# Optimization experiments

Hardware: AMD Instinct MI355X
Metric: run time of the kernel (lower is better)

Reference implementation:

```python
import jax, jax.numpy as jnp
import numpy as np

B, LQ, LK, D = 32, 1024, 1024, 256

def setup_inputs() -> dict:
    key = jax.random.key(0)
    ks = jax.random.split(key, 7)
    return {
        "raw_query": jax.random.normal(ks[0], (B, LQ, D), dtype=jnp.float32),
        "raw_key": jax.random.normal(ks[1], (B, LK, D), dtype=jnp.float32),
        "raw_value": jax.random.normal(ks[2], (B, LK, D), dtype=jnp.float32),
        "value_mask": jax.random.randint(ks[3], (B, LQ), 0, 2, dtype=jnp.int32),
        "WQ": jax.random.normal(ks[4], (D, D), dtype=jnp.float32) * 0.05,
        "WK": jax.random.normal(ks[5], (D, D), dtype=jnp.float32) * 0.05,
        "WV": jax.random.normal(ks[6], (D, D), dtype=jnp.float32) * 0.05,
    }

def reference(raw_query, raw_key, raw_value, value_mask, WQ, WK, WV):
    # Projections: [B, L, D] @ [D, D]
    Q = raw_query @ WQ
    K = raw_key @ WK
    V = raw_value @ WV
    # Scores: [B, LQ, LK] (use_scale=False -> no 1/sqrt(d_k))
    att = jnp.einsum("bqd,bkd->bqk", Q, K)
    # Mask expanded on axis=2 -> zeroes entire query rows of scores (faithful to tf.where+zeros_like)
    att = jnp.where(value_mask[:, :, None] > 0, att, jnp.zeros((), dtype=att.dtype))
    att = jax.nn.softmax(att, axis=-1)
    # Output: [B, LQ, D]
    return jnp.einsum("bqk,bkd->bqd", att, V)
```

## Files before the change

### kernel.cpp

```cpp
#include <hip/hip_runtime.h>
#include <hip/hip_bf16.h>
#include <math.h>

#define B_ 32
#define L_ 1024
#define D_ 256

typedef _Float16 half8 __attribute__((ext_vector_type(8)));
typedef __fp16   fp16x2 __attribute__((ext_vector_type(2)));
typedef short    s16x8 __attribute__((ext_vector_type(8)));
typedef float    f32x4 __attribute__((ext_vector_type(4)));

typedef __attribute__((address_space(3))) unsigned int lds_u32;
typedef __attribute__((address_space(1))) unsigned int gbl_u32;

__device__ __forceinline__ void gl_lds16(const void* g, void* l) {
    __builtin_amdgcn_global_load_lds((gbl_u32*)g, (lds_u32*)l, 16, 0, 0);
}

__device__ __forceinline__ unsigned short f2bf(float x) {
    unsigned u = __float_as_uint(x);
    u += 0x7FFFu + ((u >> 16) & 1u);
    return (unsigned short)(u >> 16);
}

__device__ __forceinline__ unsigned short f2h(float x) {
    _Float16 h = (_Float16)x;
    unsigned short u;
    __builtin_memcpy(&u, &h, 2);
    return u;
}

__device__ __forceinline__ unsigned pkrtz(float a, float b) {
    fp16x2 v = __builtin_amdgcn_cvt_pkrtz(a, b);
    unsigned u;
    __builtin_memcpy(&u, &v, 4);
    return u;
}

__global__ __launch_bounds__(256) void wprep_kernel(
    const float* __restrict__ W0, const float* __restrict__ W1,
    const float* __restrict__ W2, unsigned short* __restrict__ Wt)
{
    const int z = blockIdx.z;
    const float* __restrict__ W = (z == 0) ? W0 : (z == 1) ? W1 : W2;
    __shared__ unsigned short T[64][72];
    const int k0 = blockIdx.x << 6, n0 = blockIdx.y << 6;
    const int t = threadIdx.x;
    const int r = t >> 2, c0 = (t & 3) << 4;
    #pragma unroll
    for (int j = 0; j < 16; j += 4) {
        float4 w4 = *(const float4*)(W + (size_t)(k0 + r) * 256 + n0 + c0 + j);
        T[c0 + j + 0][r] = f2h(w4.x);
        T[c0 + j + 1][r] = f2h(w4.y);
        T[c0 + j + 2][r] = f2h(w4.z);
        T[c0 + j + 3][r] = f2h(w4.w);
    }
    __syncthreads();
    const int n = t >> 2, kc = (t & 3) << 4;
    unsigned short* dst = Wt + ((size_t)z << 16) + (size_t)(n0 + n) * 256 + k0 + kc;
    *(uint4*)(dst + 0) = *(const uint4*)&T[n][kc + 0];
    *(uint4*)(dst + 8) = *(const uint4*)&T[n][kc + 8];
}

__global__ __launch_bounds__(256) void proj_mfma_kernel(
    const float* __restrict__ A0, const float* __restrict__ A1,
    const float* __restrict__ A2, const unsigned short* __restrict__ Wt,
    unsigned short* __restrict__ Qh, unsigned short* __restrict__ Kh,
    unsigned short* __restrict__ Vt)
{
    __shared__ unsigned short SMEM[32768];
    unsigned short* Asm = SMEM;
    unsigned short* Bsm = SMEM + 16384;

    const int z = blockIdx.z;
    const float* __restrict__ A = (z == 0) ? A0 : (z == 1) ? A1 : A2;
    const int bm = blockIdx.x << 7, bn = blockIdx.y << 7;
    const int t = threadIdx.x, lane = t & 63, w = t >> 6;
    const int wm = (w >> 1) << 6, wn = (w & 1) << 6;

    const float* __restrict__ Ag = A + (size_t)bm * 256;
    const unsigned short* __restrict__ Bg = Wt + ((size_t)z << 16) + (size_t)bn * 256;

    f32x4 acc[4][4];
    const f32x4 z4 = {0.f, 0.f, 0.f, 0.f};
    #pragma unroll
    for (int mi = 0; mi < 4; ++mi)
        #pragma unroll
        for (int ni = 0; ni < 4; ++ni) acc[mi][ni] = z4;

    float4 a_reg[8];

    auto loadA = [&](int it) {
        #pragma unroll
        for (int i = 0; i < 8; ++i) {
            int r  = (t >> 4) + (i << 4);
            int c4 = t & 15;
            a_reg[i] = *(const float4*)(Ag + (size_t)r * 256 + (it << 6) + (c4 << 2));
        }
    };
    auto writeA = [&](int buf) {
        #pragma unroll
        for (int i = 0; i < 8; ++i) {
            int r  = (t >> 4) + (i << 4);
            int c4 = t & 15;
            unsigned h01 = pkrtz(a_reg[i].x, a_reg[i].y);
            unsigned h23 = pkrtz(a_reg[i].z, a_reg[i].w);
            int cs = (c4 >> 1) ^ (r & 7);
            uint2 d2; d2.x = h01; d2.y = h23;
            *(uint2*)&Asm[(buf << 13) + (r << 6) + (cs << 3) + ((c4 & 1) << 2)] = d2;
        }
    };
    auto stageB = [&](int buf, int it) {
        #pragma unroll
        for (int rr = 0; rr < 4; ++rr) {
            int o = (rr << 8) + t;
            int r = o >> 3, c = o & 7;
            int cs = c ^ (r & 7);
            gl_lds16(Bg + (size_t)r * 256 + (it << 6) + (cs << 3),
                     &Bsm[(buf << 13) + (o << 3)]);
        }
    };
    auto compute = [&](int buf) {
        #pragma unroll
        for (int kc = 0; kc < 2; ++kc) {
            half8 af[4], bfr[4];
            #pragma unroll
            for (int mi = 0; mi < 4; ++mi) {
                int m = wm + (mi << 4) + (lane & 15);
                int cs = ((kc << 2) + (lane >> 4)) ^ (m & 7);
                af[mi] = *(const half8*)&Asm[(buf << 13) + (m << 6) + (cs << 3)];
            }
            #pragma unroll
            for (int ni = 0; ni < 4; ++ni) {
                int n = wn + (ni << 4) + (lane & 15);
                int cs = ((kc << 2) + (lane >> 4)) ^ (n & 7);
                bfr[ni] = *(const half8*)&Bsm[(buf << 13) + (n << 6) + (cs << 3)];
            }
            #pragma unroll
            for (int mi = 0; mi < 4; ++mi)
                #pragma unroll
                for (int ni = 0; ni < 4; ++ni)
                    acc[mi][ni] = __builtin_amdgcn_mfma_f32_16x16x32_f16(
                        af[mi], bfr[ni], acc[mi][ni], 0, 0, 0);
        }
    };

    loadA(0);
    writeA(0);
    stageB(0, 0);
    loadA(1);
    __syncthreads();

    for (int it = 0; it < 4; ++it) {
        const int buf = it & 1;
        if (it < 3) {
            stageB(buf ^ 1, it + 1);
            writeA(buf ^ 1);
            if (it < 2) loadA(it + 2);
        }
        compute(buf);
        __syncthreads();
    }

    if (z < 2) {
        unsigned short* __restrict__ C = (z == 0) ? Qh : Kh;
        #pragma unroll
        for (int mi = 0; mi < 4; ++mi) {
            int q = bm + wm + (mi << 4) + ((lane >> 4) << 2);
            #pragma unroll
            for (int ni = 0; ni < 4; ++ni) {
                int col = bn + wn + (ni << 4) + (lane & 15);
                #pragma unroll
                for (int r = 0; r < 4; ++r)
                    C[(size_t)(q + r) * 256 + col] = f2h(acc[mi][ni][r]);
            }
        }
    } else {
        __syncthreads();
        unsigned short (*Tt)[144] = (unsigned short(*)[144])SMEM;
        #pragma unroll
        for (int mi = 0; mi < 4; ++mi) {
            #pragma unroll
            for (int ni = 0; ni < 4; ++ni) {
                int n  = wn + (ni << 4) + (lane & 15);
                int m0 = wm + (mi << 4) + ((lane >> 4) << 2);
                ushort4 v;
                v.x = f2bf(acc[mi][ni][0]);
                v.y = f2bf(acc[mi][ni][1]);
                v.z = f2bf(acc[mi][ni][2]);
                v.w = f2bf(acc[mi][ni][3]);
                *(ushort4*)&Tt[n][m0] = v;
            }
        }
        __syncthreads();
        const int bb = bm >> 10, kin = bm & 1023;
        const int dr = t >> 1, cb = (t & 1) << 6;
        unsigned short* dst = Vt + ((size_t)bb * 256 + bn + dr) * 1024 + kin + cb;
        #pragma unroll
        for (int j = 0; j < 8; ++j)
            *(uint4*)(dst + (j << 3)) = *(const uint4*)&Tt[dr][cb + (j << 3)];
    }
}

__global__ __launch_bounds__(512, 2) void fused_attn_kernel(
    const unsigned short* __restrict__ Qh, const unsigned short* __restrict__ Kh,
    const unsigned short* __restrict__ Vt, const int* __restrict__ mask,
    float* __restrict__ Out)
{
    __shared__ unsigned short Ks[2][16384];
    __shared__ unsigned short Vs[2][16384];
    __shared__ unsigned short Ps[9216];
    __shared__ float lred[128][2];

    const int b = blockIdx.y, q0 = blockIdx.x << 7;
    const size_t bL = (size_t)b * L_;
    const int t = threadIdx.x, lane = t & 63, w = t >> 6;
    const int wm_s = (w >> 1) << 5, wn_s = (w & 1) << 5;
    const int wm_v = (w >> 2) << 6, wn_v = (w & 3) << 6;

    const unsigned short* __restrict__ Kb = Kh + (bL << 8);
    const unsigned short* __restrict__ Vb = Vt + (bL << 8);

    auto stageK = [&](int buf, int kt) {
        #pragma unroll
        for (int i = 0; i < 4; ++i) {
            int o = (i << 9) + t;
            int r = o >> 5, c = o & 31;
            int cs = (c & 24) | ((c & 7) ^ (r & 7));
            gl_lds16(Kb + (size_t)((kt << 6) + r) * 256 + (cs << 3), &Ks[buf][o << 3]);
        }
    };
    auto stageV = [&](int buf, int kt) {
        #pragma unroll
        for (int i = 0; i < 4; ++i) {
            int o = (i << 9) + t;
            int d = o >> 3, c = o & 7;
            int cs = c ^ (d & 7);
            gl_lds16(Vb + ((size_t)d << 10) + (kt << 6) + (cs << 3), &Vs[buf][o << 3]);
        }
    };

    stageK(0, 0);
    stageV(0, 0);

    half8 qf[2][8];
    #pragma unroll
    for (int mi = 0; mi < 2; ++mi) {
        int m = wm_s + (mi << 4) + (lane & 15);
        const unsigned short* qp = Qh + ((bL + q0 + m) << 8) + ((lane >> 4) << 3);
        #pragma unroll
        for (int kc = 0; kc < 8; ++kc)
            qf[mi][kc] = *(const half8*)(qp + (kc << 5));
    }
    int mv[2][4];
    #pragma unroll
    for (int mi = 0; mi < 2; ++mi)
        #pragma unroll
        for (int r = 0; r < 4; ++r)
            mv[mi][r] = mask[bL + q0 + wm_s + (mi << 4) + ((lane >> 4) << 2) + r];

    f32x4 o_acc[4][4];
    const f32x4 z4 = {0.f, 0.f, 0.f, 0.f};
    #pragma unroll
    for (int mi = 0; mi < 4; ++mi)
        #pragma unroll
        for (int ni = 0; ni < 4; ++ni) o_acc[mi][ni] = z4;
    float lacc[2][4] = {};

    __syncthreads();

    for (int kt = 0; kt < 16; ++kt) {
        const int cur = kt & 1;
        if (kt < 15) { stageK(cur ^ 1, kt + 1); stageV(cur ^ 1, kt + 1); }

        f32x4 accs[2][2];
        accs[0][0] = z4; accs[0][1] = z4; accs[1][0] = z4; accs[1][1] = z4;
        #pragma unroll
        for (int kc = 0; kc < 8; ++kc) {
            int kb = (kc >> 1) << 6, cc = ((kc & 1) << 2) + (lane >> 4);
            int n0 = wn_s + (lane & 15);
            int n1 = n0 + 16;
            half8 bf0 = *(const half8*)&Ks[cur][(n0 << 8) + kb + ((cc ^ (n0 & 7)) << 3)];
            half8 bf1 = *(const half8*)&Ks[cur][(n1 << 8) + kb + ((cc ^ (n1 & 7)) << 3)];
            accs[0][0] = __builtin_amdgcn_mfma_f32_16x16x32_f16(qf[0][kc], bf0, accs[0][0], 0, 0, 0);
            accs[1][0] = __builtin_amdgcn_mfma_f32_16x16x32_f16(qf[1][kc], bf0, accs[1][0], 0, 0, 0);
            accs[0][1] = __builtin_amdgcn_mfma_f32_16x16x32_f16(qf[0][kc], bf1, accs[0][1], 0, 0, 0);
            accs[1][1] = __builtin_amdgcn_mfma_f32_16x16x32_f16(qf[1][kc], bf1, accs[1][1], 0, 0, 0);
        }

        #pragma unroll
        for (int mi = 0; mi < 2; ++mi) {
            int qrow = wm_s + (mi << 4) + ((lane >> 4) << 2);
            #pragma unroll
            for (int ni = 0; ni < 2; ++ni) {
                int kl = wn_s + (ni << 4) + (lane & 15);
                #pragma unroll
                for (int r = 0; r < 4; ++r) {
                    float p = mv[mi][r] ? __expf(accs[mi][ni][r]) : 1.0f;
                    Ps[(qrow + r) * 72 + kl] = f2bf(p);
                    lacc[mi][r] += p;
                }
            }
        }
        __syncthreads();

        #pragma unroll
        for (int kc2 = 0; kc2 < 2; ++kc2) {
            s16x8 pa[4], vb[4];
            #pragma unroll
            for (int mi = 0; mi < 4; ++mi) {
                int m = wm_v + (mi << 4) + (lane & 15);
                pa[mi] = *(const s16x8*)&Ps[m * 72 + (kc2 << 5) + ((lane >> 4) << 3)];
            }
            #pragma unroll
            for (int ni = 0; ni < 4; ++ni) {
                int n = wn_v + (ni << 4) + (lane & 15);
                int cc = (kc2 << 2) + (lane >> 4);
                vb[ni] = *(const s16x8*)&Vs[cur][(n << 6) + ((cc ^ (n & 7)) << 3)];
            }
            #pragma unroll
            for (int mi = 0; mi < 4; ++mi)
                #pragma unroll
                for (int ni = 0; ni < 4; ++ni)
                    o_acc[mi][ni] = __builtin_amdgcn_mfma_f32_16x16x32_bf16(
                        pa[mi], vb[ni], o_acc[mi][ni], 0, 0, 0);
        }
        __syncthreads();
    }

    #pragma unroll
    for (int mi = 0; mi < 2; ++mi)
        #pragma unroll
        for (int r = 0; r < 4; ++r) {
            float v = lacc[mi][r];
            v += __shfl_xor(v, 1);
            v += __shfl_xor(v, 2);
            v += __shfl_xor(v, 4);
            v += __shfl_xor(v, 8);
            if ((lane & 15) == 0)
                lred[wm_s + (mi << 4) + ((lane >> 4) << 2) + r][w & 1] = v;
        }
    __syncthreads();

    #pragma unroll
    for (int mi = 0; mi < 4; ++mi) {
        #pragma unroll
        for (int rr = 0; rr < 4; ++rr) {
            int q = wm_v + (mi << 4) + ((lane >> 4) << 2) + rr;
            float inv = 1.0f / (lred[q][0] + lred[q][1]);
            #pragma unroll
            for (int ni = 0; ni < 4; ++ni) {
                int d = wn_v + (ni << 4) + (lane & 15);
                Out[((bL + q0 + q) << 8) + d] = o_acc[mi][ni][rr] * inv;
            }
        }
    }
}

extern "C" void kernel_launch(void* const* d_in, const int* in_sizes, int n_in,
                              void* d_out, int out_size, void* d_ws, size_t ws_size,
                              hipStream_t stream) {
    const float* rq = (const float*)d_in[0];
    const float* rk = (const float*)d_in[1];
    const float* rv = (const float*)d_in[2];
    const int*   vm = (const int*)d_in[3];
    const float* WQ = (const float*)d_in[4];
    const float* WK = (const float*)d_in[5];
    const float* WV = (const float*)d_in[6];
    float* out = (float*)d_out;

    char* ws = (char*)d_ws;
    unsigned short* Qh = (unsigned short*)(ws);
    unsigned short* Kh = (unsigned short*)(ws + ((size_t)16 << 20));
    unsigned short* Vt = (unsigned short*)(ws + ((size_t)32 << 20));
    unsigned short* Wt = (unsigned short*)(ws + ((size_t)48 << 20));

    dim3 wg(4, 4, 3);
    wprep_kernel<<<wg, 256, 0, stream>>>(WQ, WK, WV, Wt);

    dim3 pg(256, 2, 3);
    proj_mfma_kernel<<<pg, 256, 0, stream>>>(rq, rk, rv, Wt, Qh, Kh, Vt);

    dim3 fg(8, 32);
    fused_attn_kernel<<<fg, 512, 0, stream>>>(Qh, Kh, Vt, vm, out);
}
```

Baseline: 98.43 us.

## Halve query tile, single-buffer K/V with split staging, remap grid for occupancy

```diff
diff --git a/kernel.cpp b/kernel.cpp
--- a/kernel.cpp
+++ b/kernel.cpp
@@ -203,113 +203,112 @@
     }
 }
 
-__global__ __launch_bounds__(512, 2) void fused_attn_kernel(
+__global__ __launch_bounds__(512, 4) void fused_attn_kernel(
     const unsigned short* __restrict__ Qh, const unsigned short* __restrict__ Kh,
     const unsigned short* __restrict__ Vt, const int* __restrict__ mask,
     float* __restrict__ Out)
 {
-    __shared__ unsigned short Ks[2][16384];
-    __shared__ unsigned short Vs[2][16384];
-    __shared__ unsigned short Ps[9216];
-    __shared__ float lred[128][2];
-
-    const int b = blockIdx.y, q0 = blockIdx.x << 7;
+    __shared__ unsigned short Ks[16384];
+    __shared__ unsigned short Vs[16384];
+    __shared__ unsigned short Ps[64 * 72];
+    __shared__ float lred[64][2];
+
+    const int f  = blockIdx.x;
+    const int b  = (f & 7) + ((f >> 7) << 3);
+    const int q0 = ((f >> 3) & 15) << 6;
     const size_t bL = (size_t)b * L_;
     const int t = threadIdx.x, lane = t & 63, w = t >> 6;
-    const int wm_s = (w >> 1) << 5, wn_s = (w & 1) << 5;
-    const int wm_v = (w >> 2) << 6, wn_v = (w & 3) << 6;
+    const int wm_s = (w >> 1) << 4, wn_s = (w & 1) << 5;
+    const int wm_v = (w >> 2) << 5, wn_v = (w & 3) << 6;
 
     const unsigned short* __restrict__ Kb = Kh + (bL << 8);
     const unsigned short* __restrict__ Vb = Vt + (bL << 8);
 
-    auto stageK = [&](int buf, int kt) {
+    auto stageK = [&](int kt) {
         #pragma unroll
         for (int i = 0; i < 4; ++i) {
             int o = (i << 9) + t;
             int r = o >> 5, c = o & 31;
             int cs = (c & 24) | ((c & 7) ^ (r & 7));
-            gl_lds16(Kb + (size_t)((kt << 6) + r) * 256 + (cs << 3), &Ks[buf][o << 3]);
-        }
-    };
-    auto stageV = [&](int buf, int kt) {
+            gl_lds16(Kb + (size_t)((kt << 6) + r) * 256 + (cs << 3), &Ks[o << 3]);
+        }
+    };
+    auto stageV = [&](int kt) {
         #pragma unroll
         for (int i = 0; i < 4; ++i) {
             int o = (i << 9) + t;
             int d = o >> 3, c = o & 7;
             int cs = c ^ (d & 7);
-            gl_lds16(Vb + ((size_t)d << 10) + (kt << 6) + (cs << 3), &Vs[buf][o << 3]);
-        }
-    };
-
-    stageK(0, 0);
-    stageV(0, 0);
-
-    half8 qf[2][8];
-    #pragma unroll
-    for (int mi = 0; mi < 2; ++mi) {
-        int m = wm_s + (mi << 4) + (lane & 15);
+            gl_lds16(Vb + ((size_t)d << 10) + (kt << 6) + (cs << 3), &Vs[o << 3]);
+        }
+    };
+
+    stageK(0);
+    stageV(0);
+
+    half8 qf[8];
+    {
+        int m = wm_s + (lane & 15);
         const unsigned short* qp = Qh + ((bL + q0 + m) << 8) + ((lane >> 4) << 3);
         #pragma unroll
         for (int kc = 0; kc < 8; ++kc)
-            qf[mi][kc] = *(const half8*)(qp + (kc << 5));
-    }
-    int mv[2][4];
+            qf[kc] = *(const half8*)(qp + (kc << 5));
+    }
+    int mv[4];
+    {
+        int qrow = wm_s + ((lane >> 4) << 2);
+        #pragma unroll
+        for (int r = 0; r < 4; ++r) mv[r] = mask[bL + q0 + qrow + r];
+    }
+
+    f32x4 o_acc[2][4];
+    const f32x4 z4 = {0.f, 0.f, 0.f, 0.f};
     #pragma unroll
     for (int mi = 0; mi < 2; ++mi)
         #pragma unroll
-        for (int r = 0; r < 4; ++r)
-            mv[mi][r] = mask[bL + q0 + wm_s + (mi << 4) + ((lane >> 4) << 2) + r];
-
-    f32x4 o_acc[4][4];
-    const f32x4 z4 = {0.f, 0.f, 0.f, 0.f};
-    #pragma unroll
-    for (int mi = 0; mi < 4; ++mi)
-        #pragma unroll
         for (int ni = 0; ni < 4; ++ni) o_acc[mi][ni] = z4;
-    float lacc[2][4] = {};
+    float lacc[4] = {};
 
     __syncthreads();
 
     for (int kt = 0; kt < 16; ++kt) {
-        const int cur = kt & 1;
-        if (kt < 15) { stageK(cur ^ 1, kt + 1); stageV(cur ^ 1, kt + 1); }
-
-        f32x4 accs[2][2];
-        accs[0][0] = z4; accs[0][1] = z4; accs[1][0] = z4; accs[1][1] = z4;
+        if (kt > 0) stageV(kt);
+
+        f32x4 accs[2];
+        accs[0] = z4; accs[1] = z4;
         #pragma unroll
         for (int kc = 0; kc < 8; ++kc) {
             int kb = (kc >> 1) << 6, cc = ((kc & 1) << 2) + (lane >> 4);
             int n0 = wn_s + (lane & 15);
             int n1 = n0 + 16;
-            half8 bf0 = *(const half8*)&Ks[cur][(n0 << 8) + kb + ((cc ^ (n0 & 7)) << 3)];
-            half8 bf1 = *(const half8*)&Ks[cur][(n1 << 8) + kb + ((cc ^ (n1 & 7)) << 3)];
-            accs[0][0] = __builtin_amdgcn_mfma_f32_16x16x32_f16(qf[0][kc], bf0, accs[0][0], 0, 0, 0);
-            accs[1][0] = __builtin_amdgcn_mfma_f32_16x16x32_f16(qf[1][kc], bf0, accs[1][0], 0, 0, 0);
-            accs[0][1] = __builtin_amdgcn_mfma_f32_16x16x32_f16(qf[0][kc], bf1, accs[0][1], 0, 0, 0);
-            accs[1][1] = __builtin_amdgcn_mfma_f32_16x16x32_f16(qf[1][kc], bf1, accs[1][1], 0, 0, 0);
-        }
-
-        #pragma unroll
-        for (int mi = 0; mi < 2; ++mi) {
-            int qrow = wm_s + (mi << 4) + ((lane >> 4) << 2);
+            half8 bf0 = *(const half8*)&Ks[(n0 << 8) + kb + ((cc ^ (n0 & 7)) << 3)];
+            half8 bf1 = *(const half8*)&Ks[(n1 << 8) + kb + ((cc ^ (n1 & 7)) << 3)];
+            accs[0] = __builtin_amdgcn_mfma_f32_16x16x32_f16(qf[kc], bf0, accs[0], 0, 0, 0);
+            accs[1] = __builtin_amdgcn_mfma_f32_16x16x32_f16(qf[kc], bf1, accs[1], 0, 0, 0);
+        }
+
+        {
+            int qrow = wm_s + ((lane >> 4) << 2);
             #pragma unroll
             for (int ni = 0; ni < 2; ++ni) {
                 int kl = wn_s + (ni << 4) + (lane & 15);
                 #pragma unroll
                 for (int r = 0; r < 4; ++r) {
-                    float p = mv[mi][r] ? __expf(accs[mi][ni][r]) : 1.0f;
+                    float p = mv[r] ? __expf(accs[ni][r]) : 1.0f;
                     Ps[(qrow + r) * 72 + kl] = f2bf(p);
-                    lacc[mi][r] += p;
+                    lacc[r] += p;
                 }
             }
         }
         __syncthreads();
 
+        if (kt < 15) stageK(kt + 1);
+
         #pragma unroll
         for (int kc2 = 0; kc2 < 2; ++kc2) {
-            s16x8 pa[4], vb[4];
-            #pragma unroll
-            for (int mi = 0; mi < 4; ++mi) {
+            s16x8 pa[2], vb[4];
+            #pragma unroll
+            for (int mi = 0; mi < 2; ++mi) {
                 int m = wm_v + (mi << 4) + (lane & 15);
                 pa[mi] = *(const s16x8*)&Ps[m * 72 + (kc2 << 5) + ((lane >> 4) << 3)];
             }
@@ -317,10 +316,10 @@
             for (int ni = 0; ni < 4; ++ni) {
                 int n = wn_v + (ni << 4) + (lane & 15);
                 int cc = (kc2 << 2) + (lane >> 4);
-                vb[ni] = *(const s16x8*)&Vs[cur][(n << 6) + ((cc ^ (n & 7)) << 3)];
-            }
-            #pragma unroll
-            for (int mi = 0; mi < 4; ++mi)
+                vb[ni] = *(const s16x8*)&Vs[(n << 6) + ((cc ^ (n & 7)) << 3)];
+            }
+            #pragma unroll
+            for (int mi = 0; mi < 2; ++mi)
                 #pragma unroll
                 for (int ni = 0; ni < 4; ++ni)
                     o_acc[mi][ni] = __builtin_amdgcn_mfma_f32_16x16x32_bf16(
@@ -330,21 +329,19 @@
     }
 
     #pragma unroll
-    for (int mi = 0; mi < 2; ++mi)
-        #pragma unroll
-        for (int r = 0; r < 4; ++r) {
-            float v = lacc[mi][r];
-            v += __shfl_xor(v, 1);
-            v += __shfl_xor(v, 2);
-            v += __shfl_xor(v, 4);
-            v += __shfl_xor(v, 8);
-            if ((lane & 15) == 0)
-                lred[wm_s + (mi << 4) + ((lane >> 4) << 2) + r][w & 1] = v;
-        }
+    for (int r = 0; r < 4; ++r) {
+        float v = lacc[r];
+        v += __shfl_xor(v, 1);
+        v += __shfl_xor(v, 2);
+        v += __shfl_xor(v, 4);
+        v += __shfl_xor(v, 8);
+        if ((lane & 15) == 0)
+            lred[wm_s + ((lane >> 4) << 2) + r][w & 1] = v;
+    }
     __syncthreads();
 
     #pragma unroll
-    for (int mi = 0; mi < 4; ++mi) {
+    for (int mi = 0; mi < 2; ++mi) {
         #pragma unroll
         for (int rr = 0; rr < 4; ++rr) {
             int q = wm_v + (mi << 4) + ((lane >> 4) << 2) + rr;
@@ -382,6 +379,5 @@
     dim3 pg(256, 2, 3);
     proj_mfma_kernel<<<pg, 256, 0, stream>>>(rq, rk, rv, Wt, Qh, Kh, Vt);
 
-    dim3 fg(8, 32);
-    fused_attn_kernel<<<fg, 512, 0, stream>>>(Qh, Kh, Vt, vm, out);
-}
+    fused_attn_kernel<<<512, 512, 0, stream>>>(Qh, Kh, Vt, vm, out);
+}
```

After: 100.6 us. 2.2% more time.

## Single-buffer K/V tiles, swizzle P tile, remap grid for XCD locality

Applied to the files above, without the earlier changes.

```diff
diff --git a/kernel.cpp b/kernel.cpp
--- a/kernel.cpp
+++ b/kernel.cpp
@@ -203,17 +203,19 @@
     }
 }
 
-__global__ __launch_bounds__(512, 2) void fused_attn_kernel(
+__global__ __launch_bounds__(512, 4) void fused_attn_kernel(
     const unsigned short* __restrict__ Qh, const unsigned short* __restrict__ Kh,
     const unsigned short* __restrict__ Vt, const int* __restrict__ mask,
     float* __restrict__ Out)
 {
-    __shared__ unsigned short Ks[2][16384];
-    __shared__ unsigned short Vs[2][16384];
-    __shared__ unsigned short Ps[9216];
-    __shared__ float lred[128][2];
-
-    const int b = blockIdx.y, q0 = blockIdx.x << 7;
+    __shared__ unsigned short Ks[16384];
+    __shared__ unsigned short Vs[16384];
+    __shared__ unsigned short Ps[128 * 64];
+    float* lredp = (float*)Ps;
+
+    const int f  = blockIdx.x;
+    const int b  = (f & 7) + ((f >> 6) << 3);
+    const int q0 = ((f >> 3) & 7) << 7;
     const size_t bL = (size_t)b * L_;
     const int t = threadIdx.x, lane = t & 63, w = t >> 6;
     const int wm_s = (w >> 1) << 5, wn_s = (w & 1) << 5;
@@ -222,27 +224,27 @@
     const unsigned short* __restrict__ Kb = Kh + (bL << 8);
     const unsigned short* __restrict__ Vb = Vt + (bL << 8);
 
-    auto stageK = [&](int buf, int kt) {
+    auto stageK = [&](int kt) {
         #pragma unroll
         for (int i = 0; i < 4; ++i) {
             int o = (i << 9) + t;
             int r = o >> 5, c = o & 31;
             int cs = (c & 24) | ((c & 7) ^ (r & 7));
-            gl_lds16(Kb + (size_t)((kt << 6) + r) * 256 + (cs << 3), &Ks[buf][o << 3]);
-        }
-    };
-    auto stageV = [&](int buf, int kt) {
+            gl_lds16(Kb + (size_t)((kt << 6) + r) * 256 + (cs << 3), &Ks[o << 3]);
+        }
+    };
+    auto stageV = [&](int kt) {
         #pragma unroll
         for (int i = 0; i < 4; ++i) {
             int o = (i << 9) + t;
             int d = o >> 3, c = o & 7;
             int cs = c ^ (d & 7);
-            gl_lds16(Vb + ((size_t)d << 10) + (kt << 6) + (cs << 3), &Vs[buf][o << 3]);
-        }
-    };
-
-    stageK(0, 0);
-    stageV(0, 0);
+            gl_lds16(Vb + ((size_t)d << 10) + (kt << 6) + (cs << 3), &Vs[o << 3]);
+        }
+    };
+
+    stageK(0);
+    stageV(0);
 
     half8 qf[2][8];
     #pragma unroll
@@ -271,8 +273,7 @@
     __syncthreads();
 
     for (int kt = 0; kt < 16; ++kt) {
-        const int cur = kt & 1;
-        if (kt < 15) { stageK(cur ^ 1, kt + 1); stageV(cur ^ 1, kt + 1); }
+        if (kt > 0) stageV(kt);
 
         f32x4 accs[2][2];
         accs[0][0] = z4; accs[0][1] = z4; accs[1][0] = z4; accs[1][1] = z4;
@@ -281,8 +282,8 @@
             int kb = (kc >> 1) << 6, cc = ((kc & 1) << 2) + (lane >> 4);
             int n0 = wn_s + (lane & 15);
             int n1 = n0 + 16;
-            half8 bf0 = *(const half8*)&Ks[cur][(n0 << 8) + kb + ((cc ^ (n0 & 7)) << 3)];
-            half8 bf1 = *(const half8*)&Ks[cur][(n1 << 8) + kb + ((cc ^ (n1 & 7)) << 3)];
+            half8 bf0 = *(const half8*)&Ks[(n0 << 8) + kb + ((cc ^ (n0 & 7)) << 3)];
+            half8 bf1 = *(const half8*)&Ks[(n1 << 8) + kb + ((cc ^ (n1 & 7)) << 3)];
             accs[0][0] = __builtin_amdgcn_mfma_f32_16x16x32_f16(qf[0][kc], bf0, accs[0][0], 0, 0, 0);
             accs[1][0] = __builtin_amdgcn_mfma_f32_16x16x32_f16(qf[1][kc], bf0, accs[1][0], 0, 0, 0);
             accs[0][1] = __builtin_amdgcn_mfma_f32_16x16x32_f16(qf[0][kc], bf1, accs[0][1], 0, 0, 0);
@@ -297,27 +298,31 @@
                 int kl = wn_s + (ni << 4) + (lane & 15);
                 #pragma unroll
                 for (int r = 0; r < 4; ++r) {
+                    int q = qrow + r;
                     float p = mv[mi][r] ? __expf(accs[mi][ni][r]) : 1.0f;
-                    Ps[(qrow + r) * 72 + kl] = f2bf(p);
+                    Ps[(q << 6) + ((((kl >> 3) ^ (q & 7)) << 3)) + (kl & 7)] = f2bf(p);
                     lacc[mi][r] += p;
                 }
             }
         }
         __syncthreads();
 
+        if (kt < 15) stageK(kt + 1);
+
         #pragma unroll
         for (int kc2 = 0; kc2 < 2; ++kc2) {
             s16x8 pa[4], vb[4];
             #pragma unroll
             for (int mi = 0; mi < 4; ++mi) {
                 int m = wm_v + (mi << 4) + (lane & 15);
-                pa[mi] = *(const s16x8*)&Ps[m * 72 + (kc2 << 5) + ((lane >> 4) << 3)];
+                int c0 = (kc2 << 2) + (lane >> 4);
+                pa[mi] = *(const s16x8*)&Ps[(m << 6) + ((c0 ^ (m & 7)) << 3)];
             }
             #pragma unroll
             for (int ni = 0; ni < 4; ++ni) {
                 int n = wn_v + (ni << 4) + (lane & 15);
                 int cc = (kc2 << 2) + (lane >> 4);
-                vb[ni] = *(const s16x8*)&Vs[cur][(n << 6) + ((cc ^ (n & 7)) << 3)];
+                vb[ni] = *(const s16x8*)&Vs[(n << 6) + ((cc ^ (n & 7)) << 3)];
             }
             #pragma unroll
             for (int mi = 0; mi < 4; ++mi)
@@ -339,7 +344,7 @@
             v += __shfl_xor(v, 4);
             v += __shfl_xor(v, 8);
             if ((lane & 15) == 0)
-                lred[wm_s + (mi << 4) + ((lane >> 4) << 2) + r][w & 1] = v;
+                lredp[((wm_s + (mi << 4) + ((lane >> 4) << 2) + r) << 1) + (w & 1)] = v;
         }
     __syncthreads();
 
@@ -348,7 +353,7 @@
         #pragma unroll
         for (int rr = 0; rr < 4; ++rr) {
             int q = wm_v + (mi << 4) + ((lane >> 4) << 2) + rr;
-            float inv = 1.0f / (lred[q][0] + lred[q][1]);
+            float inv = 1.0f / (lredp[q << 1] + lredp[(q << 1) + 1]);
             #pragma unroll
             for (int ni = 0; ni < 4; ++ni) {
                 int d = wn_v + (ni << 4) + (lane & 15);
@@ -382,6 +387,5 @@
     dim3 pg(256, 2, 3);
     proj_mfma_kernel<<<pg, 256, 0, stream>>>(rq, rk, rv, Wt, Qh, Kh, Vt);
 
-    dim3 fg(8, 32);
-    fused_attn_kernel<<<fg, 512, 0, stream>>>(Qh, Kh, Vt, vm, out);
-}
+    fused_attn_kernel<<<256, 512, 0, stream>>>(Qh, Kh, Vt, vm, out);
+}
```

Result: slower. 260.0 us (+164.1%).
